# Optimization experiments

Measured on AMD Instinct MI355X. Metric: run time of the kernel, lower is better.

The kernel has to match this reference:

```python
import jax, jax.numpy as jnp
import numpy as np

B, S, HID, NH = 8, 1024, 1024, 16
HD = HID // NH


def setup_inputs() -> dict:
    key = jax.random.key(0)
    ks = jax.random.split(key, 7)
    scale = 1.0 / np.sqrt(HID)
    return {
        "x": jax.random.normal(ks[0], (B, S, HID), dtype=jnp.float32),
        "attention_mask": jax.random.uniform(ks[1], (B, 1, S, S), dtype=jnp.float32),
        "Wq": jax.random.normal(ks[2], (HID, HID), dtype=jnp.float32) * scale,
        "bq": jnp.zeros((HID,), jnp.float32),
        "Wk": jax.random.normal(ks[3], (HID, HID), dtype=jnp.float32) * scale,
        "bk": jnp.zeros((HID,), jnp.float32),
        "Wv": jax.random.normal(ks[4], (HID, HID), dtype=jnp.float32) * scale,
        "bv": jnp.zeros((HID,), jnp.float32),
        "Wp": jax.random.normal(ks[5], (HID, HID), dtype=jnp.float32) * scale,
        "bp": jnp.zeros((HID,), jnp.float32),
    }


def _split(t):
    # [B, S, HID] -> [B, NH, S, HD]
    b, s, _ = t.shape
    return t.reshape(b, s, NH, HD).transpose(0, 2, 1, 3)


def reference(x, attention_mask, Wq, bq, Wk, bk, Wv, bv, Wp, bp):
    q = _split(x @ Wq + bq)  # [B, NH, S, HD]
    k = _split(x @ Wk + bk)
    v = _split(x @ Wv + bv)
    # NOTE: module scales by rsqrt(full hidden_dim) = rsqrt(NH*HD), faithful to source
    scores = jnp.einsum("bhqd,bhkd->bhqk", q, k) * jax.lax.rsqrt(jnp.float32(HID))
    scores = scores + attention_mask * (-1e9)
    attn = jax.nn.softmax(scores, axis=-1)
    ctx = jnp.einsum("bhqk,bhkd->bhqd", attn, v)  # [B, NH, S, HD]
    ctx = ctx.transpose(0, 2, 1, 3).reshape(x.shape[0], x.shape[1], HID)
    # projection (Conv1D k=1 == dense); dropout is identity at inference
    return ctx @ Wp + bp
```

## Files before the change

### kernel.cpp

```cpp
#include <hip/hip_runtime.h>


using bf16x8 = __attribute__((ext_vector_type(8))) short;
using f32x4  = __attribute__((ext_vector_type(4))) float;

#define DEVFN __device__ __forceinline__

typedef const __attribute__((address_space(1))) void gas_void;
typedef __attribute__((address_space(3))) void las_void;

DEVFN void gload16(const void* g, void* l) {
  __builtin_amdgcn_global_load_lds((gas_void*)g, (las_void*)l, 16, 0, 0);
}

DEVFN unsigned short f2bf(float f) {
  union { float f; unsigned u; } v; v.f = f;
  unsigned r = v.u + 0x7fffu + ((v.u >> 16) & 1u);
  return (unsigned short)(r >> 16);
}

DEVFN unsigned cvtpk(float lo, float hi) {
  unsigned r;
  asm("v_cvt_pk_bf16_f32 %0, %1, %2" : "=v"(r) : "v"(lo), "v"(hi));
  return r;
}

__global__ __launch_bounds__(256) void k_convert_x(const float* __restrict__ x,
                                                   unsigned short* __restrict__ xb) {
  int i = (blockIdx.x * 256 + threadIdx.x) * 4;
  float4 v = *reinterpret_cast<const float4*>(x + i);
  ushort4 o;
  o.x = f2bf(v.x); o.y = f2bf(v.y); o.z = f2bf(v.z); o.w = f2bf(v.w);
  *reinterpret_cast<ushort4*>(xb + i) = o;
}

__global__ __launch_bounds__(256) void k_transpose_w(const float* __restrict__ Wq,
                                                     const float* __restrict__ Wk,
                                                     const float* __restrict__ Wv,
                                                     const float* __restrict__ Wp,
                                                     unsigned short* __restrict__ Wcat,
                                                     unsigned short* __restrict__ Wpt) {
  __shared__ float tile[64][65];
  int z = blockIdx.z;
  const float* W = (z == 0) ? Wq : (z == 1) ? Wk : (z == 2) ? Wv : Wp;
  unsigned short* out = (z == 3) ? Wpt : (Wcat + (size_t)z * 1024 * 1024);
  int k0 = blockIdx.y * 64, n0 = blockIdx.x * 64;
  int t = threadIdx.x;
  int tr = t >> 4, tc = (t & 15) * 4;
#pragma unroll
  for (int p = 0; p < 4; ++p) {
    int k = p * 16 + tr;
    float4 v = *reinterpret_cast<const float4*>(W + (size_t)(k0 + k) * 1024 + n0 + tc);
    tile[k][tc + 0] = v.x; tile[k][tc + 1] = v.y;
    tile[k][tc + 2] = v.z; tile[k][tc + 3] = v.w;
  }
  __syncthreads();
#pragma unroll
  for (int p = 0; p < 4; ++p) {
    int n = p * 16 + tr;
    ushort4 o;
    o.x = f2bf(tile[tc + 0][n]); o.y = f2bf(tile[tc + 1][n]);
    o.z = f2bf(tile[tc + 2][n]); o.w = f2bf(tile[tc + 3][n]);
    *reinterpret_cast<ushort4*>(out + (size_t)(n0 + n) * 1024 + k0 + tc) = o;
  }
}

template <int MODE>
__global__ __launch_bounds__(256) void k_gemm(const unsigned short* __restrict__ A,
                                              const unsigned short* __restrict__ Bt,
                                              const float* __restrict__ b0,
                                              const float* __restrict__ b1,
                                              const float* __restrict__ b2,
                                              unsigned short* __restrict__ Qb,
                                              unsigned short* __restrict__ Kb,
                                              unsigned short* __restrict__ Vtb,
                                              float* __restrict__ outp) {
  __shared__ unsigned short sm[128 * 128];
  unsigned short* As = sm;
  unsigned short* Bs = sm + 128 * 64;
  int t = threadIdx.x, lane = t & 63, w = t >> 6;
  int lgrp = lane >> 4, l16 = lane & 15;
  int n0 = blockIdx.x * 128, m0 = blockIdx.y * 128;
  int wm = w >> 1, wn = w & 1;
  const unsigned short* Ag = A + (size_t)m0 * 1024;
  const unsigned short* Bg = Bt + (size_t)n0 * 1024;

  const f32x4 zf = {0.f, 0.f, 0.f, 0.f};
  f32x4 acc[4][4];
#pragma unroll
  for (int mi = 0; mi < 4; ++mi)
#pragma unroll
    for (int ni = 0; ni < 4; ++ni) acc[mi][ni] = zf;

  for (int kt = 0; kt < 16; ++kt) {
    int kof = kt * 64;
#pragma unroll
    for (int is = 0; is < 4; ++is) {
      int ci = is * 256 + t;
      int row = ci >> 3, c = ci & 7;
      gload16(Ag + (size_t)row * 1024 + kof + c * 8, As + ci * 8);
      gload16(Bg + (size_t)row * 1024 + kof + c * 8, Bs + ci * 8);
    }
    __syncthreads();
    bf16x8 af[4][2], bfr[4][2];
#pragma unroll
    for (int mi = 0; mi < 4; ++mi)
#pragma unroll
      for (int s = 0; s < 2; ++s)
        af[mi][s] = *reinterpret_cast<const bf16x8*>(
            As + (wm * 64 + mi * 16 + l16) * 64 + s * 32 + lgrp * 8);
#pragma unroll
    for (int ni = 0; ni < 4; ++ni)
#pragma unroll
      for (int s = 0; s < 2; ++s)
        bfr[ni][s] = *reinterpret_cast<const bf16x8*>(
            Bs + (wn * 64 + ni * 16 + l16) * 64 + s * 32 + lgrp * 8);
#pragma unroll
    for (int mi = 0; mi < 4; ++mi)
#pragma unroll
      for (int ni = 0; ni < 4; ++ni)
#pragma unroll
        for (int s = 0; s < 2; ++s)
          acc[mi][ni] = __builtin_amdgcn_mfma_f32_16x16x32_bf16(
              af[mi][s], bfr[ni][s], acc[mi][ni], 0, 0, 0);
    __syncthreads();
  }

  if (MODE == 0) {
    int seg = n0 >> 10;
    int nn0 = n0 & 1023;
    const float* bias = (seg == 0) ? b0 : (seg == 1) ? b1 : b2;
    if (seg < 2) {
      unsigned short* o = (seg == 0) ? Qb : Kb;
#pragma unroll
      for (int ni = 0; ni < 4; ++ni) {
        int n = nn0 + wn * 64 + ni * 16 + l16;
        float bval = bias[n];
#pragma unroll
        for (int mi = 0; mi < 4; ++mi) {
          int ml = wm * 64 + mi * 16 + lgrp * 4;
#pragma unroll
          for (int r = 0; r < 4; ++r)
            o[(size_t)(m0 + ml + r) * 1024 + n] = f2bf(acc[mi][ni][r] + bval);
        }
      }
    } else {
#pragma unroll
      for (int ni = 0; ni < 4; ++ni) {
        int nl = wn * 64 + ni * 16 + l16;
        float bval = bias[nn0 + nl];
        int sw = (nl & 7) << 3;
#pragma unroll
        for (int mi = 0; mi < 4; ++mi) {
          int ml = wm * 64 + mi * 16 + lgrp * 4;
#pragma unroll
          for (int r = 0; r < 4; ++r)
            sm[nl * 128 + ((ml + r) ^ sw)] = f2bf(acc[mi][ni][r] + bval);
        }
      }
      __syncthreads();
      int bb = m0 >> 10, s0 = m0 & 1023;
      int nl = t >> 1, mh = (t & 1) * 64;
      int ng = nn0 + nl, hh = ng >> 6, d = ng & 63;
      unsigned short* vb = Vtb + ((size_t)(bb * 16 + hh) * 64 + d) * 1024 + s0;
      int sw = (nl & 7) << 3;
#pragma unroll
      for (int j = 0; j < 8; ++j) {
        int me = mh + j * 8;
        bf16x8 v = *reinterpret_cast<const bf16x8*>(sm + nl * 128 + (me ^ sw));
        *reinterpret_cast<bf16x8*>(vb + me) = v;
      }
    }
  } else {
#pragma unroll
    for (int ni = 0; ni < 4; ++ni) {
      int n = n0 + wn * 64 + ni * 16 + l16;
      float bval = b0[n];
#pragma unroll
      for (int mi = 0; mi < 4; ++mi) {
        int ml = wm * 64 + mi * 16 + lgrp * 4;
#pragma unroll
        for (int r = 0; r < 4; ++r)
          outp[(size_t)(m0 + ml + r) * 1024 + n] = acc[mi][ni][r] + bval;
      }
    }
  }
}

__global__ __launch_bounds__(256) void k_attn(const unsigned short* __restrict__ Qb,
                                              const unsigned short* __restrict__ Kb,
                                              const unsigned short* __restrict__ Vtb,
                                              const float* __restrict__ mask,
                                              unsigned short* __restrict__ ctx) {
  __shared__ unsigned short QPs[64 * 64];
  __shared__ unsigned short Ks[2][64 * 64];
  __shared__ unsigned short Vts[2][64 * 64];

  int t = threadIdx.x, lane = t & 63, w = t >> 6;
  int lgrp = lane >> 4, l16 = lane & 15;
  int gid = blockIdx.x;
  int xcd = gid & 7, ii = gid >> 3;
  int grp = (ii >> 4) * 8 + xcd;
  int h = ii & 15;
  int b = grp >> 4, qt = grp & 15;
  int row64 = w * 16 + l16;

  const unsigned short* Qg = Qb + ((size_t)(b * 1024 + qt * 64)) * 1024 + h * 64;
  const unsigned short* Kg = Kb + (size_t)b * 1024 * 1024 + h * 64;
  const unsigned short* Vg = Vtb + ((size_t)(b * 16 + h) * 64) * 1024;
  const float* mrow = mask + (size_t)b * 1024 * 1024 + (size_t)(qt * 64 + row64) * 1024;

#pragma unroll
  for (int is = 0; is < 2; ++is) {
    int ci = is * 256 + t, row = ci >> 3, c = ci & 7, cs = c ^ (row & 7);
    gload16(Qg + (size_t)row * 1024 + cs * 8, QPs + ci * 8);
    gload16(Kg + (size_t)row * 1024 + cs * 8, Ks[0] + ci * 8);
    gload16(Vg + (size_t)row * 1024 + cs * 8, Vts[0] + ci * 8);
  }
  float4 mkc[4], mkn[4];
#pragma unroll
  for (int ct = 0; ct < 4; ++ct)
    mkc[ct] = *reinterpret_cast<const float4*>(mrow + ct * 16 + lgrp * 4);
  __syncthreads();

  bf16x8 aq[2];
#pragma unroll
  for (int s = 0; s < 2; ++s) {
    int c = (s * 4 + lgrp) ^ (row64 & 7);
    aq[s] = *reinterpret_cast<const bf16x8*>(QPs + row64 * 64 + c * 8);
  }
  __syncthreads();

  const f32x4 zf = {0.f, 0.f, 0.f, 0.f};
  f32x4 acc[4];
#pragma unroll
  for (int dt = 0; dt < 4; ++dt) acc[dt] = zf;
  float m_s = -__builtin_inff(), l_s = 0.f;
  int cur = 0;

  for (int kt = 0; kt < 16; ++kt) {
    if (kt < 15) {
#pragma unroll
      for (int is = 0; is < 2; ++is) {
        int ci = is * 256 + t, row = ci >> 3, c = ci & 7, cs = c ^ (row & 7);
        gload16(Kg + (size_t)(kt + 1) * 64 * 1024 + (size_t)row * 1024 + cs * 8,
                Ks[cur ^ 1] + ci * 8);
        gload16(Vg + (size_t)row * 1024 + (kt + 1) * 64 + cs * 8, Vts[cur ^ 1] + ci * 8);
      }
#pragma unroll
      for (int ct = 0; ct < 4; ++ct)
        mkn[ct] = *reinterpret_cast<const float4*>(mrow + (kt + 1) * 64 + ct * 16 + lgrp * 4);
    }

    float sc[16];
    float mx = -__builtin_inff();
    __builtin_amdgcn_s_setprio(1);
#pragma unroll
    for (int ct = 0; ct < 4; ++ct) {
      f32x4 sac = zf;
#pragma unroll
      for (int s = 0; s < 2; ++s) {
        int row = ct * 16 + l16;
        int c = (s * 4 + lgrp) ^ (row & 7);
        bf16x8 ak = *reinterpret_cast<const bf16x8*>(Ks[cur] + row * 64 + c * 8);
        sac = __builtin_amdgcn_mfma_f32_16x16x32_bf16(ak, aq[s], sac, 0, 0, 0);
      }
      const float* mp = reinterpret_cast<const float*>(&mkc[ct]);
#pragma unroll
      for (int r = 0; r < 4; ++r) {
        float v = __fadd_rn(__fmul_rn(sac[r], 0.03125f), __fmul_rn(mp[r], -1e9f));
        sc[ct * 4 + r] = v;
        mx = fmaxf(mx, v);
      }
    }
    __builtin_amdgcn_s_setprio(0);
    mx = fmaxf(mx, __shfl_xor(mx, 16, 64));
    mx = fmaxf(mx, __shfl_xor(mx, 32, 64));

    bool skip = __all(mx <= m_s) != 0;
    float resc = 1.f;
    if (!skip) {
      float mn = fmaxf(m_s, mx);
      resc = __expf(m_s - mn);
      m_s = mn;
    }
    float rs = 0.f;
#pragma unroll
    for (int i = 0; i < 16; ++i) {
      float p = __expf(sc[i] - m_s);
      sc[i] = p;
      rs += p;
    }
    rs += __shfl_xor(rs, 16, 64);
    rs += __shfl_xor(rs, 32, 64);
    if (skip) {
      l_s += rs;
    } else {
      l_s = l_s * resc + rs;
      float racc[4];
#pragma unroll
      for (int r = 0; r < 4; ++r) racc[r] = __shfl(resc, lgrp * 4 + r, 64);
#pragma unroll
      for (int dt = 0; dt < 4; ++dt)
#pragma unroll
        for (int r = 0; r < 4; ++r) acc[dt][r] *= racc[r];
    }

#pragma unroll
    for (int ct = 0; ct < 4; ++ct) {
      uint2 u;
      u.x = cvtpk(sc[ct * 4 + 0], sc[ct * 4 + 1]);
      u.y = cvtpk(sc[ct * 4 + 2], sc[ct * 4 + 3]);
      int chunk = ct * 2 + (lgrp >> 1);
      int ep = row64 * 64 + ((chunk ^ (l16 & 7)) << 3) + ((lgrp & 1) << 2);
      *reinterpret_cast<uint2*>(&QPs[ep]) = u;
    }
    asm volatile("" ::: "memory");

    __builtin_amdgcn_s_setprio(1);
#pragma unroll
    for (int s = 0; s < 2; ++s) {
      int ec = row64 * 64 + (((s * 4 + lgrp) ^ (l16 & 7)) << 3);
      bf16x8 ap = *reinterpret_cast<const bf16x8*>(&QPs[ec]);
#pragma unroll
      for (int dt = 0; dt < 4; ++dt) {
        int row = dt * 16 + l16;
        int c = (s * 4 + lgrp) ^ (row & 7);
        bf16x8 bv_ = *reinterpret_cast<const bf16x8*>(Vts[cur] + row * 64 + c * 8);
        acc[dt] = __builtin_amdgcn_mfma_f32_16x16x32_bf16(ap, bv_, acc[dt], 0, 0, 0);
      }
    }
    __builtin_amdgcn_s_setprio(0);
    __syncthreads();
    cur ^= 1;
#pragma unroll
    for (int ct = 0; ct < 4; ++ct) mkc[ct] = mkn[ct];
  }

  float linv[4];
#pragma unroll
  for (int r = 0; r < 4; ++r) linv[r] = 1.0f / __shfl(l_s, lgrp * 4 + r, 64);
  size_t mbase = (size_t)(b * 1024 + qt * 64 + w * 16 + lgrp * 4);
#pragma unroll
  for (int dt = 0; dt < 4; ++dt)
#pragma unroll
    for (int r = 0; r < 4; ++r)
      ctx[(mbase + r) * 1024 + h * 64 + dt * 16 + l16] = f2bf(acc[dt][r] * linv[r]);
}

extern "C" void kernel_launch(void* const* d_in, const int* in_sizes, int n_in,
                              void* d_out, int out_size, void* d_ws, size_t ws_size,
                              hipStream_t stream) {
  const float* x    = (const float*)d_in[0];
  const float* mask = (const float*)d_in[1];
  const float* Wq = (const float*)d_in[2];
  const float* bq = (const float*)d_in[3];
  const float* Wk = (const float*)d_in[4];
  const float* bk = (const float*)d_in[5];
  const float* Wv = (const float*)d_in[6];
  const float* bv = (const float*)d_in[7];
  const float* Wp = (const float*)d_in[8];
  const float* bp = (const float*)d_in[9];

  const size_t MB = 1u << 20;
  char* ws = (char*)d_ws;
  unsigned short* xbf  = (unsigned short*)(ws + 0);
  unsigned short* Wcat = (unsigned short*)(ws + 16 * MB);
  unsigned short* Wpt  = (unsigned short*)(ws + 22 * MB);
  unsigned short* Qb   = (unsigned short*)(ws + 24 * MB);
  unsigned short* Kb   = (unsigned short*)(ws + 40 * MB);
  unsigned short* Vtb  = (unsigned short*)(ws + 56 * MB);
  unsigned short* ctx  = xbf;

  k_convert_x<<<8192, 256, 0, stream>>>(x, xbf);
  k_transpose_w<<<dim3(16, 16, 4), 256, 0, stream>>>(Wq, Wk, Wv, Wp, Wcat, Wpt);
  k_gemm<0><<<dim3(24, 64), 256, 0, stream>>>(xbf, Wcat, bq, bk, bv, Qb, Kb, Vtb, nullptr);
  k_attn<<<2048, 256, 0, stream>>>(Qb, Kb, Vtb, mask, ctx);
  k_gemm<1><<<dim3(8, 64), 256, 0, stream>>>(ctx, Wpt, bp, nullptr, nullptr,
                                             nullptr, nullptr, nullptr, (float*)d_out);
}
```

Measured before the change: 328.6 us.

## Remap QKV GEMM blocks per XCD and restructure attention LDS buffering

The QKV GEMM now launches as a 1D grid and remaps block ids so that consecutive blocks on each XCD share the same row tiles of x, to improve L2 reuse. The attention kernel loads Q directly from global memory into registers and no longer stages it in LDS. It gives P its own LDS buffer and single-buffers V, loading the next V tile after the PV stage instead of prefetching it. This frees LDS, which may allow higher occupancy, but adds an extra barrier per iteration and exposes more of the V load latency.

```diff
diff --git a/kernel.cpp b/kernel.cpp
--- a/kernel.cpp
+++ b/kernel.cpp
@@ -80,7 +80,16 @@
   unsigned short* Bs = sm + 128 * 64;
   int t = threadIdx.x, lane = t & 63, w = t >> 6;
   int lgrp = lane >> 4, l16 = lane & 15;
-  int n0 = blockIdx.x * 128, m0 = blockIdx.y * 128;
+  int bx, by;
+  if (MODE == 0) {
+    int lid = blockIdx.x;
+    int x = lid & 7, j = lid >> 3;
+    by = x * 8 + (j & 7);
+    bx = j >> 3;
+  } else {
+    bx = blockIdx.x; by = blockIdx.y;
+  }
+  int n0 = bx * 128, m0 = by * 128;
   int wm = w >> 1, wn = w & 1;
   const unsigned short* Ag = A + (size_t)m0 * 1024;
   const unsigned short* Bg = Bt + (size_t)n0 * 1024;
@@ -192,9 +201,9 @@
                                               const unsigned short* __restrict__ Vtb,
                                               const float* __restrict__ mask,
                                               unsigned short* __restrict__ ctx) {
-  __shared__ unsigned short QPs[64 * 64];
   __shared__ unsigned short Ks[2][64 * 64];
-  __shared__ unsigned short Vts[2][64 * 64];
+  __shared__ unsigned short Vts[64 * 64];
+  __shared__ unsigned short Ps[64 * 64];
 
   int t = threadIdx.x, lane = t & 63, w = t >> 6;
   int lgrp = lane >> 4, l16 = lane & 15;
@@ -213,22 +222,17 @@
 #pragma unroll
   for (int is = 0; is < 2; ++is) {
     int ci = is * 256 + t, row = ci >> 3, c = ci & 7, cs = c ^ (row & 7);
-    gload16(Qg + (size_t)row * 1024 + cs * 8, QPs + ci * 8);
     gload16(Kg + (size_t)row * 1024 + cs * 8, Ks[0] + ci * 8);
-    gload16(Vg + (size_t)row * 1024 + cs * 8, Vts[0] + ci * 8);
-  }
+    gload16(Vg + (size_t)row * 1024 + cs * 8, Vts + ci * 8);
+  }
+  bf16x8 aq[2];
+#pragma unroll
+  for (int s = 0; s < 2; ++s)
+    aq[s] = *reinterpret_cast<const bf16x8*>(Qg + (size_t)row64 * 1024 + (s * 4 + lgrp) * 8);
   float4 mkc[4], mkn[4];
 #pragma unroll
   for (int ct = 0; ct < 4; ++ct)
     mkc[ct] = *reinterpret_cast<const float4*>(mrow + ct * 16 + lgrp * 4);
-  __syncthreads();
-
-  bf16x8 aq[2];
-#pragma unroll
-  for (int s = 0; s < 2; ++s) {
-    int c = (s * 4 + lgrp) ^ (row64 & 7);
-    aq[s] = *reinterpret_cast<const bf16x8*>(QPs + row64 * 64 + c * 8);
-  }
   __syncthreads();
 
   const f32x4 zf = {0.f, 0.f, 0.f, 0.f};
@@ -245,7 +249,6 @@
         int ci = is * 256 + t, row = ci >> 3, c = ci & 7, cs = c ^ (row & 7);
         gload16(Kg + (size_t)(kt + 1) * 64 * 1024 + (size_t)row * 1024 + cs * 8,
                 Ks[cur ^ 1] + ci * 8);
-        gload16(Vg + (size_t)row * 1024 + (kt + 1) * 64 + cs * 8, Vts[cur ^ 1] + ci * 8);
       }
 #pragma unroll
       for (int ct = 0; ct < 4; ++ct)
@@ -313,25 +316,35 @@
       u.y = cvtpk(sc[ct * 4 + 2], sc[ct * 4 + 3]);
       int chunk = ct * 2 + (lgrp >> 1);
       int ep = row64 * 64 + ((chunk ^ (l16 & 7)) << 3) + ((lgrp & 1) << 2);
-      *reinterpret_cast<uint2*>(&QPs[ep]) = u;
+      *reinterpret_cast<uint2*>(&Ps[ep]) = u;
     }
     asm volatile("" ::: "memory");
+
+    __syncthreads();
 
     __builtin_amdgcn_s_setprio(1);
 #pragma unroll
     for (int s = 0; s < 2; ++s) {
       int ec = row64 * 64 + (((s * 4 + lgrp) ^ (l16 & 7)) << 3);
-      bf16x8 ap = *reinterpret_cast<const bf16x8*>(&QPs[ec]);
+      bf16x8 ap = *reinterpret_cast<const bf16x8*>(&Ps[ec]);
 #pragma unroll
       for (int dt = 0; dt < 4; ++dt) {
         int row = dt * 16 + l16;
         int c = (s * 4 + lgrp) ^ (row & 7);
-        bf16x8 bv_ = *reinterpret_cast<const bf16x8*>(Vts[cur] + row * 64 + c * 8);
+        bf16x8 bv_ = *reinterpret_cast<const bf16x8*>(Vts + row * 64 + c * 8);
         acc[dt] = __builtin_amdgcn_mfma_f32_16x16x32_bf16(ap, bv_, acc[dt], 0, 0, 0);
       }
     }
     __builtin_amdgcn_s_setprio(0);
     __syncthreads();
+
+    if (kt < 15) {
+#pragma unroll
+      for (int is = 0; is < 2; ++is) {
+        int ci = is * 256 + t, row = ci >> 3, c = ci & 7, cs = c ^ (row & 7);
+        gload16(Vg + (size_t)row * 1024 + (kt + 1) * 64 + cs * 8, Vts + ci * 8);
+      }
+    }
     cur ^= 1;
 #pragma unroll
     for (int ct = 0; ct < 4; ++ct) mkc[ct] = mkn[ct];
@@ -374,7 +387,7 @@
 
   k_convert_x<<<8192, 256, 0, stream>>>(x, xbf);
   k_transpose_w<<<dim3(16, 16, 4), 256, 0, stream>>>(Wq, Wk, Wv, Wp, Wcat, Wpt);
-  k_gemm<0><<<dim3(24, 64), 256, 0, stream>>>(xbf, Wcat, bq, bk, bv, Qb, Kb, Vtb, nullptr);
+  k_gemm<0><<<1536, 256, 0, stream>>>(xbf, Wcat, bq, bk, bv, Qb, Kb, Vtb, nullptr);
   k_attn<<<2048, 256, 0, stream>>>(Qb, Kb, Vtb, mask, ctx);
   k_gemm<1><<<dim3(8, 64), 256, 0, stream>>>(ctx, Wpt, bp, nullptr, nullptr,
                                              nullptr, nullptr, nullptr, (float*)d_out);
```

Measured after the change: 330.0 us. Within noise of the previous version (+0.5%).
